# Kernel optimization log

Hardware: AMD Instinct MI355X
Metric: run time of the kernel (lower is better)

Reference implementation:

```python
import jax, jax.numpy as jnp
import numpy as np

FI_BIT, FI_GROUP = 8, 64
FW_BIT, FW_GROUP = 8, 64


def quantize_bfp(x, bit, group):
    """Block-floating-point quantize: groups of `group` elems along the last dim
    share the exponent of the group max; mantissas are rounded to `bit` bits."""
    shp = x.shape
    xg = x.reshape(shp[:-1] + (shp[-1] // group, group))
    maxabs = jnp.max(jnp.abs(xg), axis=-1, keepdims=True)
    e = jnp.floor(jnp.log2(jnp.maximum(maxabs, jnp.asarray(1e-38, x.dtype))))
    step = jnp.exp2(e - (bit - 1))  # quantization step for shared exponent e
    qmax = 2 ** (bit - 1) - 1
    q = jnp.clip(jnp.round(xg / step), -(qmax + 1), qmax) * step
    q = jnp.where(maxabs == 0, jnp.zeros_like(q), q)
    return q.reshape(shp)


def setup_inputs() -> dict:
    key = jax.random.key(0)
    k1, k2, k3 = jax.random.split(key, 3)
    N, IN, OUT = 4096, 4096, 4096
    x = jax.random.normal(k1, (N, IN), dtype=jnp.float32)
    # weight/bias initialized uniform(-0.1, 0.1) as in the torch module
    weight = jax.random.uniform(k2, (OUT, IN), dtype=jnp.float32, minval=-0.1, maxval=0.1)
    bias = jax.random.uniform(k3, (OUT,), dtype=jnp.float32, minval=-0.1, maxval=0.1)
    return {"x": x, "weight": weight, "bias": bias}


def reference(x, weight, bias):
    xq = quantize_bfp(x, FI_BIT, FI_GROUP)          # [N, IN]
    wq = quantize_bfp(weight, FW_BIT, FW_GROUP)     # [OUT, IN]
    out = jnp.einsum('ni,oi->no', xq, wq)
    # Faithful to the original forward: F.linear adds bias once, then the
    # explicit `output += bias` adds it a second time.
    out = out + 2.0 * bias[None, :]
    return out
```

## Files before the change

kernel.cpp:

```cpp
#include <hip/hip_runtime.h>
#include <stdint.h>

typedef __bf16 bf16_t;
typedef __attribute__((ext_vector_type(8))) __bf16 bf16x8;
typedef __attribute__((ext_vector_type(4))) float f32x4;

#define NDIM 4096

__global__ __launch_bounds__(256) void quant_bfp(const float* __restrict__ in0,
                                                 bf16_t* __restrict__ out0,
                                                 const float* __restrict__ in1,
                                                 bf16_t* __restrict__ out1) {
    const float* in = blockIdx.y ? in1 : in0;
    bf16_t* out     = blockIdx.y ? out1 : out0;
    const int stride = gridDim.x * 256;
    for (int t = blockIdx.x * 256 + threadIdx.x; t < NDIM * NDIM / 4; t += stride) {
        float4 v = ((const float4*)in)[t];
        float m = fmaxf(fmaxf(fabsf(v.x), fabsf(v.y)), fmaxf(fabsf(v.z), fabsf(v.w)));
        m = fmaxf(m, __shfl_xor(m, 1));
        m = fmaxf(m, __shfl_xor(m, 2));
        m = fmaxf(m, __shfl_xor(m, 4));
        m = fmaxf(m, __shfl_xor(m, 8));
        const int e = (int)((__float_as_uint(m) >> 23) & 0xFF) - 127;
        float step = __uint_as_float((uint32_t)(e + 120) << 23);
        float inv  = __uint_as_float((uint32_t)(134 - e) << 23);
        if (m == 0.0f) { step = 0.0f; inv = 0.0f; }
        float q0 = fminf(fmaxf(rintf(v.x * inv), -128.0f), 127.0f) * step;
        float q1 = fminf(fmaxf(rintf(v.y * inv), -128.0f), 127.0f) * step;
        float q2 = fminf(fmaxf(rintf(v.z * inv), -128.0f), 127.0f) * step;
        float q3 = fminf(fmaxf(rintf(v.w * inv), -128.0f), 127.0f) * step;
        union { bf16_t b[4]; uint2 u; } o;
        o.b[0] = (bf16_t)q0; o.b[1] = (bf16_t)q1;
        o.b[2] = (bf16_t)q2; o.b[3] = (bf16_t)q3;
        ((uint2*)out)[t] = o.u;
    }
}

__device__ __forceinline__ void g2l16(const bf16_t* g, void* l) {
    __builtin_amdgcn_global_load_lds(
        (__attribute__((address_space(1))) void*)g,
        (__attribute__((address_space(3))) void*)l, 16, 0, 0);
}

#define FENCE() asm volatile("" ::: "memory")
#define BAR()   do { FENCE(); __builtin_amdgcn_sched_barrier(0);              \
                     __builtin_amdgcn_s_barrier();                            \
                     __builtin_amdgcn_sched_barrier(0); FENCE(); } while (0)
#define WAITV(n) asm volatile("s_waitcnt vmcnt(" #n ")" ::: "memory")
#define LGKM8()  asm volatile("s_waitcnt lgkmcnt(8)" ::: "memory")

#define STAGE_A(b, h, ko) do {                                                  \
    g2l16(gA + (size_t)((h) * 128) * NDIM + (ko),                               \
          (char*)sA + (b) * 32768 + (h) * 16384 + tid * 16);                    \
    g2l16(gA + (size_t)((h) * 128 + 64) * NDIM + (ko),                          \
          (char*)sA + (b) * 32768 + (h) * 16384 + 8192 + tid * 16);             \
} while (0)
#define STAGE_B(b, h, ko) do {                                                  \
    g2l16(gB + (size_t)((h) * 128) * NDIM + (ko),                               \
          (char*)sB + (b) * 32768 + (h) * 16384 + tid * 16);                    \
    g2l16(gB + (size_t)((h) * 128 + 64) * NDIM + (ko),                          \
          (char*)sB + (b) * 32768 + (h) * 16384 + 8192 + tid * 16);             \
} while (0)

#define LDA(b, qm) do {                                                         \
    _Pragma("unroll")                                                           \
    for (int i_ = 0; i_ < 4; ++i_) {                                            \
        const int r_ = (b) * 16384 + aRow + ((qm) * 64 + i_ * 16) * 64;         \
        afr[i_][0] = *(const bf16x8*)&sA[r_ + ce0];                             \
        afr[i_][1] = *(const bf16x8*)&sA[r_ + ce1];                             \
    }                                                                           \
} while (0)
#define LDB(b, qn) do {                                                         \
    _Pragma("unroll")                                                           \
    for (int j_ = 0; j_ < 2; ++j_) {                                            \
        const int r_ = (b) * 16384 + bRow + ((qn) * 32 + j_ * 16) * 64;         \
        bfr[qn][j_][0] = *(const bf16x8*)&sB[r_ + ce0];                         \
        bfr[qn][j_][1] = *(const bf16x8*)&sB[r_ + ce1];                         \
    }                                                                           \
} while (0)

#define MFMAQ(qm, qn) do {                                                      \
    __builtin_amdgcn_s_setprio(1);                                              \
    _Pragma("unroll")                                                           \
    for (int i_ = 0; i_ < 4; ++i_)                                              \
        _Pragma("unroll")                                                       \
        for (int j_ = 0; j_ < 2; ++j_) {                                        \
            acc[(qm)*4+i_][(qn)*2+j_] = __builtin_amdgcn_mfma_f32_16x16x32_bf16(\
                afr[i_][0], bfr[qn][j_][0], acc[(qm)*4+i_][(qn)*2+j_], 0, 0, 0);\
            acc[(qm)*4+i_][(qn)*2+j_] = __builtin_amdgcn_mfma_f32_16x16x32_bf16(\
                afr[i_][1], bfr[qn][j_][1], acc[(qm)*4+i_][(qn)*2+j_], 0, 0, 0);\
        }                                                                       \
    __builtin_amdgcn_s_setprio(0);                                              \
} while (0)

__global__ __launch_bounds__(512, 2) void gemm_bfp(const bf16_t* __restrict__ A,
                                                   const bf16_t* __restrict__ B,
                                                   const float* __restrict__ bias,
                                                   float* __restrict__ C) {
    __shared__ bf16_t sA[2 * 256 * 64];
    __shared__ bf16_t sB[2 * 256 * 64];

    const int tid  = threadIdx.x;
    const int wave = tid >> 6;
    const int lane = tid & 63;
    const int wr   = wave >> 2;
    const int wc   = wave & 3;

    const int p  = blockIdx.x;
    const int wg = (p & 7) * 32 + (p >> 3);
    const int bm = wg >> 4;
    const int bn = wg & 15;

    const int srow = tid >> 3;
    const int swz  = ((tid & 7) ^ (srow & 7)) * 8;
    const bf16_t* gA = A + (size_t)(bm * 256 + srow) * NDIM + swz;
    const bf16_t* gB = B + (size_t)(bn * 256 + srow) * NDIM + swz;

    const int quad = lane >> 4;
    const int l16  = lane & 15;
    const int rsw  = l16 & 7;
    const int ce0  = (quad ^ rsw) * 8;
    const int ce1  = ((4 + quad) ^ rsw) * 8;
    const int aRow = (wr * 128 + l16) * 64;
    const int bRow = (wc * 64 + l16) * 64;

    f32x4 acc[8][4];
#pragma unroll
    for (int i = 0; i < 8; ++i)
#pragma unroll
        for (int j = 0; j < 4; ++j) acc[i][j] = (f32x4){0.0f, 0.0f, 0.0f, 0.0f};

    bf16x8 afr[4][2];
    bf16x8 bfr[2][2][2];

    STAGE_A(0, 0, 0); STAGE_A(0, 1, 0);
    STAGE_B(0, 0, 0); STAGE_B(0, 1, 0);
    STAGE_B(1, 0, 64); STAGE_B(1, 1, 64);
    WAITV(0);
    BAR();

    for (int kt = 0; kt < NDIM; kt += 128) {
        const int koA1 = kt + 64;
        const int koN2 = (kt + 128 < NDIM) ? kt + 128 : 0;
        const int koB3 = (kt + 192 < NDIM) ? kt + 192 : 0;

        LDA(0, 0); LDB(0, 0);
        STAGE_A(1, 0, koA1);
        LGKM8();
        BAR();
        MFMAQ(0, 0);
        BAR();

        LDB(0, 1);
        STAGE_A(1, 1, koA1);
        BAR();
        MFMAQ(0, 1);
        BAR();

        LDA(0, 1);
        STAGE_B(0, 0, koN2);
        BAR();
        MFMAQ(1, 1);
        BAR();

        STAGE_B(0, 1, koN2);
        BAR();
        MFMAQ(1, 0);
        WAITV(4);
        BAR();

        LDA(1, 0); LDB(1, 0);
        STAGE_A(0, 0, koN2);
        LGKM8();
        BAR();
        MFMAQ(0, 0);
        BAR();

        LDB(1, 1);
        STAGE_A(0, 1, koN2);
        BAR();
        MFMAQ(0, 1);
        BAR();

        LDA(1, 1);
        STAGE_B(1, 0, koB3);
        BAR();
        MFMAQ(1, 1);
        BAR();

        STAGE_B(1, 1, koB3);
        BAR();
        MFMAQ(1, 0);
        WAITV(4);
        BAR();
    }

    const int row0 = bm * 256 + wr * 128 + quad * 4;
    const int col0 = bn * 256 + wc * 64 + l16;
#pragma unroll
    for (int nj = 0; nj < 4; ++nj) {
        const int c = col0 + nj * 16;
        const float bv = 2.0f * bias[c];
#pragma unroll
        for (int mi = 0; mi < 8; ++mi) {
            const int r = row0 + mi * 16;
#pragma unroll
            for (int reg = 0; reg < 4; ++reg)
                C[(size_t)(r + reg) * NDIM + c] = acc[mi][nj][reg] + bv;
        }
    }
}

extern "C" void kernel_launch(void* const* d_in, const int* in_sizes, int n_in,
                              void* d_out, int out_size, void* d_ws, size_t ws_size,
                              hipStream_t stream) {
    const float* x    = (const float*)d_in[0];
    const float* w    = (const float*)d_in[1];
    const float* bias = (const float*)d_in[2];
    float* out = (float*)d_out;

    bf16_t* xq = (bf16_t*)d_ws;
    bf16_t* wq = xq + (size_t)NDIM * NDIM;

    dim3 qgrid(1024, 2);
    quant_bfp<<<qgrid, 256, 0, stream>>>(x, xq, w, wq);

    dim3 grid(256);
    gemm_bfp<<<grid, 512, 0, stream>>>(xq, wq, bias, out);
}
```

Measured before the change: 286.2 us.

## Reorganize LDS quarter layout to release A halves earlier and deepen prefetch

Reorganizes the shared-memory layout of A and B tiles so each quarter-subtile used by an MFMA phase occupies a contiguous LDS region, letting A halves be restaged as soon as their quarter is consumed. This moves A prefetches one phase earlier and raises the outstanding-load count (WAITV 6) to overlap global loads more deeply with MFMA. It also switches output stores to nontemporal stores to avoid polluting cache. The risk is subtle buffer-reuse hazards and wave-to-row mapping changes that must remain consistent with the epilogue indexing.

```diff
diff --git a/kernel.cpp b/kernel.cpp
--- a/kernel.cpp
+++ b/kernel.cpp
@@ -49,23 +49,23 @@
 #define WAITV(n) asm volatile("s_waitcnt vmcnt(" #n ")" ::: "memory")
 #define LGKM8()  asm volatile("s_waitcnt lgkmcnt(8)" ::: "memory")
 
-#define STAGE_A(b, h, ko) do {                                                  \
-    g2l16(gA + (size_t)((h) * 128) * NDIM + (ko),                               \
-          (char*)sA + (b) * 32768 + (h) * 16384 + tid * 16);                    \
-    g2l16(gA + (size_t)((h) * 128 + 64) * NDIM + (ko),                          \
-          (char*)sA + (b) * 32768 + (h) * 16384 + 8192 + tid * 16);             \
-} while (0)
-#define STAGE_B(b, h, ko) do {                                                  \
-    g2l16(gB + (size_t)((h) * 128) * NDIM + (ko),                               \
-          (char*)sB + (b) * 32768 + (h) * 16384 + tid * 16);                    \
-    g2l16(gB + (size_t)((h) * 128 + 64) * NDIM + (ko),                          \
-          (char*)sB + (b) * 32768 + (h) * 16384 + 8192 + tid * 16);             \
+#define STAGE_A(b, r, ko) do {                                                  \
+    g2l16(gA + (size_t)((r) * 64) * NDIM + (ko),                                \
+          (char*)sA + (b) * 32768 + (r) * 16384 + tid * 16);                    \
+    g2l16(gA + (size_t)((r) * 64 + 128) * NDIM + (ko),                          \
+          (char*)sA + (b) * 32768 + (r) * 16384 + 8192 + tid * 16);             \
+} while (0)
+#define STAGE_B(b, r, ko) do {                                                  \
+    g2l16(gB + (size_t)((r) * 32) * NDIM + (ko),                                \
+          (char*)sB + (b) * 32768 + (r) * 16384 + tid * 16);                    \
+    g2l16(gB + (size_t)((r) * 32 + 128) * NDIM + (ko),                          \
+          (char*)sB + (b) * 32768 + (r) * 16384 + 8192 + tid * 16);             \
 } while (0)
 
 #define LDA(b, qm) do {                                                         \
     _Pragma("unroll")                                                           \
     for (int i_ = 0; i_ < 4; ++i_) {                                            \
-        const int r_ = (b) * 16384 + aRow + ((qm) * 64 + i_ * 16) * 64;         \
+        const int r_ = (b) * 16384 + (qm) * 8192 + aRow + i_ * 1024;            \
         afr[i_][0] = *(const bf16x8*)&sA[r_ + ce0];                             \
         afr[i_][1] = *(const bf16x8*)&sA[r_ + ce1];                             \
     }                                                                           \
@@ -73,7 +73,7 @@
 #define LDB(b, qn) do {                                                         \
     _Pragma("unroll")                                                           \
     for (int j_ = 0; j_ < 2; ++j_) {                                            \
-        const int r_ = (b) * 16384 + bRow + ((qn) * 32 + j_ * 16) * 64;         \
+        const int r_ = (b) * 16384 + (qn) * 8192 + bRow + j_ * 1024;            \
         bfr[qn][j_][0] = *(const bf16x8*)&sB[r_ + ce0];                         \
         bfr[qn][j_][1] = *(const bf16x8*)&sB[r_ + ce1];                         \
     }                                                                           \
@@ -114,15 +114,15 @@
     const int srow = tid >> 3;
     const int swz  = ((tid & 7) ^ (srow & 7)) * 8;
     const bf16_t* gA = A + (size_t)(bm * 256 + srow) * NDIM + swz;
-    const bf16_t* gB = B + (size_t)(bn * 256 + srow) * NDIM + swz;
+    const bf16_t* gB = B + (size_t)(bn * 256 + (srow >> 5) * 64 + (srow & 31)) * NDIM + swz;
 
     const int quad = lane >> 4;
     const int l16  = lane & 15;
     const int rsw  = l16 & 7;
     const int ce0  = (quad ^ rsw) * 8;
     const int ce1  = ((4 + quad) ^ rsw) * 8;
-    const int aRow = (wr * 128 + l16) * 64;
-    const int bRow = (wc * 64 + l16) * 64;
+    const int aRow = (wr * 64 + l16) * 64;
+    const int bRow = (wc * 32 + l16) * 64;
 
     f32x4 acc[8][4];
 #pragma unroll
@@ -133,10 +133,9 @@
     bf16x8 afr[4][2];
     bf16x8 bfr[2][2][2];
 
-    STAGE_A(0, 0, 0); STAGE_A(0, 1, 0);
-    STAGE_B(0, 0, 0); STAGE_B(0, 1, 0);
-    STAGE_B(1, 0, 64); STAGE_B(1, 1, 64);
-    WAITV(0);
+    STAGE_A(0, 0, 0); STAGE_B(0, 0, 0); STAGE_B(0, 1, 0); STAGE_A(0, 1, 0);
+    STAGE_A(1, 0, 64); STAGE_B(1, 0, 64); STAGE_B(1, 1, 64);
+    WAITV(6);
     BAR();
 
     for (int kt = 0; kt < NDIM; kt += 128) {
@@ -145,14 +144,14 @@
         const int koB3 = (kt + 192 < NDIM) ? kt + 192 : 0;
 
         LDA(0, 0); LDB(0, 0);
-        STAGE_A(1, 0, koA1);
+        STAGE_A(1, 1, koA1);
         LGKM8();
         BAR();
         MFMAQ(0, 0);
         BAR();
 
         LDB(0, 1);
-        STAGE_A(1, 1, koA1);
+        STAGE_A(0, 0, koN2);
         BAR();
         MFMAQ(0, 1);
         BAR();
@@ -166,18 +165,18 @@
         STAGE_B(0, 1, koN2);
         BAR();
         MFMAQ(1, 0);
-        WAITV(4);
+        WAITV(6);
         BAR();
 
         LDA(1, 0); LDB(1, 0);
-        STAGE_A(0, 0, koN2);
+        STAGE_A(0, 1, koN2);
         LGKM8();
         BAR();
         MFMAQ(0, 0);
         BAR();
 
         LDB(1, 1);
-        STAGE_A(0, 1, koN2);
+        STAGE_A(1, 0, koB3);
         BAR();
         MFMAQ(0, 1);
         BAR();
@@ -191,7 +190,7 @@
         STAGE_B(1, 1, koB3);
         BAR();
         MFMAQ(1, 0);
-        WAITV(4);
+        WAITV(6);
         BAR();
     }
 
@@ -206,7 +205,8 @@
             const int r = row0 + mi * 16;
 #pragma unroll
             for (int reg = 0; reg < 4; ++reg)
-                C[(size_t)(r + reg) * NDIM + c] = acc[mi][nj][reg] + bv;
+                __builtin_nontemporal_store(acc[mi][nj][reg] + bv,
+                                            &C[(size_t)(r + reg) * NDIM + c]);
         }
     }
 }
```

Measured after the change: 285.9 us. Within noise of the previous version (-0.1%).
